# Kernel tuning notes

Hardware: AMD Instinct MI355X
Metric: run time of the kernel (lower is better)

The kernel has to match this reference:

```python
import jax, jax.numpy as jnp
import numpy as np

def _dct_mat():
    k = np.arange(8)[:, None]
    n = np.arange(8)[None, :]
    norm = np.where(k == 0, np.sqrt(1.0 / 8.0), np.sqrt(2.0 / 8.0))
    return jnp.asarray(norm * np.cos(np.pi / 8.0 * (n + 0.5) * k), jnp.float32)

_LUM = np.array([[16,11,10,16,24,40,51,61],[12,12,14,19,26,58,60,55],[14,13,16,24,40,57,69,56],[14,17,22,29,51,87,80,62],[18,22,37,56,68,109,103,77],[24,35,55,64,81,104,113,92],[49,64,78,87,103,121,120,101],[72,92,95,98,112,100,103,99]], np.float32)
_CHROM = np.array([[17,18,24,47,99,99,99,99],[18,21,26,66,99,99,99,99],[24,26,56,99,99,99,99,99],[47,66,99,99,99,99,99,99],[99,99,99,99,99,99,99,99],[99,99,99,99,99,99,99,99],[99,99,99,99,99,99,99,99],[99,99,99,99,99,99,99,99]], np.float32)

def _qtables(quality):
    q = max(1, min(100, int(quality)))
    scale = 5000.0 / q if q < 50 else 200.0 - 2.0 * q
    tbs = np.stack([_LUM, _CHROM]) * scale
    tbs = np.clip((tbs + 50.0) / 100.0, 1.0, 255.0)
    return jnp.asarray(tbs, jnp.float32)

def _jpeg_forward(img, quality):
    bs, _, oh, ow = img.shape
    x = img * 255.0
    pad_h = (8 - oh % 8) % 8
    pad_w = (8 - ow % 8) % 8
    if pad_h or pad_w:
        x = jnp.pad(x, ((0, 0), (0, 0), (0, pad_h), (0, pad_w)), mode='edge')
    h, w = oh + pad_h, ow + pad_w
    W_ycc = jnp.asarray([[0.299, 0.587, 0.114], [-0.1687, -0.3313, 0.5], [0.5, -0.4187, -0.0813]], jnp.float32)
    b_ycc = jnp.asarray([0.0, 128.0, 128.0], jnp.float32)
    # 1x1 conv colorspace transform
    yuv = jnp.einsum('oc,bchw->bohw', W_ycc, x) + b_ycc[None, :, None, None]
    nb = bs * 3
    hb, wb = h // 8, w // 8
    # unfold(kernel=8, stride=8) == non-overlapping 8x8 blocking, block-row-major
    blocks = yuv.reshape(nb, hb, 8, wb, 8).transpose(0, 1, 3, 2, 4).reshape(nb, hb * wb, 8, 8)
    M = _dct_mat()
    dct = jnp.matmul(M, jnp.matmul(blocks - 128.0, M.T))
    qt = _qtables(quality)
    # faithful to original slicing patches_dct[:bs] / [bs:] over the flattened (b,c) dim
    row = jnp.arange(nb)[:, None, None, None]
    qfull = jnp.where(row < bs, qt[0], qt[1])
    t = dct / qfull
    # straight-through round
    tq = (t + jax.lax.stop_gradient(jnp.round(t) - t)) * qfull
    idct = jnp.matmul(M.T, jnp.matmul(tq, M)) + 128.0
    rec = idct.reshape(nb, hb, wb, 8, 8).transpose(0, 1, 3, 2, 4).reshape(bs, 3, h, w)
    rec = rec - b_ycc[None, :, None, None]
    y, cb, cr = rec[:, 0], rec[:, 1], rec[:, 2]
    r = y + 1.402 * cr
    g = y - 0.34414 * cb - 0.71414 * cr
    b = y + 1.772 * cb
    rgb = jnp.stack([r, g, b], axis=1)[:, :, :oh, :ow]
    return jnp.clip(rgb / 255.0, 0.0, 1.0)

def setup_inputs() -> dict:
    key = jax.random.key(0)
    img = jax.random.uniform(key, (16, 3, 512, 512), dtype=jnp.float32)
    return {"img": img, "quality": 80}

def reference(img, quality):
    return _jpeg_forward(img, quality)
```

## Files before the change

### kernel.cpp

```cpp
#include <hip/hip_runtime.h>
#include <math.h>

#define C1 0.9807852804032304
#define C2 0.9238795325112867
#define C3 0.8314696123025452
#define C4 0.7071067811865476
#define C5 0.5555702330196022
#define C6 0.3826834323650898
#define C7 0.19509032201612825
#define N0 0.35355339059327373

static constexpr double Mc[8][8] = {
 {  N0,      N0,      N0,      N0,      N0,      N0,      N0,      N0    },
 {  .5*C1,   .5*C3,   .5*C5,   .5*C7,  -.5*C7,  -.5*C5,  -.5*C3,  -.5*C1 },
 {  .5*C2,   .5*C6,  -.5*C6,  -.5*C2,  -.5*C2,  -.5*C6,   .5*C6,   .5*C2 },
 {  .5*C3,  -.5*C7,  -.5*C1,  -.5*C5,   .5*C5,   .5*C1,   .5*C7,  -.5*C3 },
 {  .5*C4,  -.5*C4,  -.5*C4,   .5*C4,   .5*C4,  -.5*C4,  -.5*C4,   .5*C4 },
 {  .5*C5,  -.5*C1,   .5*C7,   .5*C3,  -.5*C3,  -.5*C7,   .5*C1,  -.5*C5 },
 {  .5*C6,  -.5*C2,   .5*C2,  -.5*C6,  -.5*C6,   .5*C2,  -.5*C2,   .5*C6 },
 {  .5*C7,  -.5*C5,   .5*C3,  -.5*C1,   .5*C1,  -.5*C3,   .5*C5,  -.5*C7 },
};
#define ROWF(r) {(float)Mc[r][0],(float)Mc[r][1],(float)Mc[r][2],(float)Mc[r][3],\
                 (float)Mc[r][4],(float)Mc[r][5],(float)Mc[r][6],(float)Mc[r][7]}
static constexpr float Mcf[8][8] = {ROWF(0),ROWF(1),ROWF(2),ROWF(3),ROWF(4),ROWF(5),ROWF(6),ROWF(7)};

static __device__ const double LUM_BASE[64] = {
 16,11,10,16,24,40,51,61,
 12,12,14,19,26,58,60,55,
 14,13,16,24,40,57,69,56,
 14,17,22,29,51,87,80,62,
 18,22,37,56,68,109,103,77,
 24,35,55,64,81,104,113,92,
 49,64,78,87,103,121,120,101,
 72,92,95,98,112,100,103,99};
static __device__ const double CHROM_BASE[64] = {
 17,18,24,47,99,99,99,99,
 18,21,26,66,99,99,99,99,
 24,26,56,99,99,99,99,99,
 47,66,99,99,99,99,99,99,
 99,99,99,99,99,99,99,99,
 99,99,99,99,99,99,99,99,
 99,99,99,99,99,99,99,99,
 99,99,99,99,99,99,99,99};

__global__ __launch_bounds__(192, 4) void jpeg_fwd(const float* __restrict__ img,
                                                   const int* __restrict__ quality,
                                                   float* __restrict__ out)
{
    __shared__ double QT[128];
    __shared__ double RQ[128];
    __shared__ double U[1728];

    const int t   = threadIdx.x;
    const int w   = t >> 6;
    const int l   = t & 63;
    const int blk = l >> 3;
    const int rr  = l & 7;

    const int b    = blockIdx.x >> 9;
    const int rem  = blockIdx.x & 511;
    const int row0 = (rem >> 3) << 3;
    const int col0 = (rem & 7) << 6;

    const size_t plane = 512 * 512;

    const float* p = img + (size_t)(b * 3) * plane + (size_t)(row0 + rr) * 512 + col0 + blk * 8;
    float4 R0 = *(const float4*)(p);
    float4 R1 = *(const float4*)(p + 4);
    float4 G0 = *(const float4*)(p + plane);
    float4 G1 = *(const float4*)(p + plane + 4);
    float4 B0 = *(const float4*)(p + 2 * plane);
    float4 B1 = *(const float4*)(p + 2 * plane + 4);

    {
        int q = quality[0];
        q = q < 1 ? 1 : (q > 100 ? 100 : q);
        double scale = (q < 50) ? (5000.0 / (double)q) : (200.0 - 2.0 * (double)q);
        #pragma unroll
        for (int h = 0; h < 2; ++h) {
            int e = l + (h << 6);
            int tbl = e >> 6, idx = e & 63;
            double base = tbl ? CHROM_BASE[idx] : LUM_BASE[idx];
            double v = (base * scale + 50.0) / 100.0;
            v = fmin(fmax(v, 1.0), 255.0);
            QT[e] = v;
            RQ[e] = 1.0 / v;
        }
    }

    const double F00 =  0.299 * 255.0,  F01 =  0.587 * 255.0,  F02 =  0.114 * 255.0;
    const double F10 = -0.1687 * 255.0, F11 = -0.3313 * 255.0, F12 =  0.5 * 255.0;
    const double F20 =  0.5 * 255.0,    F21 = -0.4187 * 255.0, F22 = -0.0813 * 255.0;

    float rf[8] = {R0.x, R0.y, R0.z, R0.w, R1.x, R1.y, R1.z, R1.w};
    float gf[8] = {G0.x, G0.y, G0.z, G0.w, G1.x, G1.y, G1.z, G1.w};
    float bf[8] = {B0.x, B0.y, B0.z, B0.w, B1.x, B1.y, B1.z, B1.w};

    double row[8];
    #pragma unroll
    for (int k = 0; k < 8; ++k) {
        double rv = (double)rf[k];
        double gv = (double)gf[k];
        double bv = (double)bf[k];
        double v;
        if (w == 0)      v = F00 * rv + F01 * gv + F02 * bv;
        else if (w == 1) v = F10 * rv + F11 * gv + F12 * bv + 128.0;
        else             v = F20 * rv + F21 * gv + F22 * bv + 128.0;
        row[k] = v - 128.0;
    }

    double y[8];
    {
        double u0[4], v0[4];
        #pragma unroll
        for (int k = 0; k < 4; ++k) {
            u0[k] = row[k] + row[7 - k];
            v0[k] = row[k] - row[7 - k];
        }
        #pragma unroll
        for (int c = 0; c < 8; c += 2) {
            double se = 0.0, so = 0.0;
            #pragma unroll
            for (int k = 0; k < 4; ++k) {
                se += u0[k] * Mc[c][k];
                so += v0[k] * Mc[c + 1][k];
            }
            y[c] = se; y[c + 1] = so;
        }
    }

    {
        double* tb = U + w * 576 + blk * 72 + rr * 9;
        #pragma unroll
        for (int k = 0; k < 8; ++k) tb[k] = y[k];
    }
    double t1[8], qv[8], rv8[8];
    {
        const double* tb = U + w * 576 + blk * 72 + rr;
        #pragma unroll
        for (int k = 0; k < 8; ++k) t1[k] = tb[k * 9];
    }
    const int sel = ((b * 3 + w) < 16) ? 0 : 1;
    #pragma unroll
    for (int j = 0; j < 8; ++j) {
        qv[j]  = QT[(sel << 6) + (j << 3) + rr];
        rv8[j] = RQ[(sel << 6) + (j << 3) + rr];
    }

    double wq[8];
    {
        double tu[4], tv[4];
        #pragma unroll
        for (int k = 0; k < 4; ++k) {
            tu[k] = t1[k] + t1[7 - k];
            tv[k] = t1[k] - t1[7 - k];
        }
        #pragma unroll
        for (int j = 0; j < 8; j += 2) {
            double se = 0.0, so = 0.0;
            #pragma unroll
            for (int k = 0; k < 4; ++k) {
                se += tu[k] * Mc[j][k];
                so += tv[k] * Mc[j + 1][k];
            }
            {
                double q = qv[j], r = rv8[j];
                double qh = se * r;
                double e  = fma(-q, qh, se);
                double qq = fma(e, r, qh);
                wq[j] = rint(qq) * q;
            }
            {
                double q = qv[j + 1], r = rv8[j + 1];
                double qh = so * r;
                double e  = fma(-q, qh, so);
                double qq = fma(e, r, qh);
                wq[j + 1] = rint(qq) * q;
            }
        }
    }

    float wqf[8];
    #pragma unroll
    for (int k = 0; k < 8; ++k) wqf[k] = (float)wq[k];

    float a3[8];
    #pragma unroll
    for (int j = 0; j < 4; ++j) {
        float pe = 0.0f, po = 0.0f;
        #pragma unroll
        for (int k = 0; k < 4; ++k) {
            pe += wqf[2 * k]     * Mcf[2 * k][j];
            po += wqf[2 * k + 1] * Mcf[2 * k + 1][j];
        }
        a3[j]     = pe + po;
        a3[7 - j] = pe - po;
    }

    {
        float* tb = (float*)(U + w * 576) + blk * 72 + rr * 9;
        #pragma unroll
        for (int k = 0; k < 8; ++k) tb[k] = a3[k];
    }
    __syncthreads();

    float tY[8], tU[8], tV[8];
    {
        const float* c0 = (float*)(U + 0 * 576) + blk * 72 + rr;
        const float* c1 = (float*)(U + 1 * 576) + blk * 72 + rr;
        const float* c2 = (float*)(U + 2 * 576) + blk * 72 + rr;
        #pragma unroll
        for (int k = 0; k < 8; ++k) {
            tY[k] = c0[k * 9];
            tU[k] = c1[k * 9];
            tV[k] = c2[k * 9];
        }
    }

    float yr[8], ur[8], vr[8];
    #pragma unroll
    for (int j = 0; j < 4; ++j) {
        float eY = 0.0f, oY = 0.0f, eU = 0.0f, oU = 0.0f, eV = 0.0f, oV = 0.0f;
        #pragma unroll
        for (int k = 0; k < 4; ++k) {
            float me = Mcf[2 * k][j], mo = Mcf[2 * k + 1][j];
            eY += tY[2 * k] * me;  oY += tY[2 * k + 1] * mo;
            eU += tU[2 * k] * me;  oU += tU[2 * k + 1] * mo;
            eV += tV[2 * k] * me;  oV += tV[2 * k + 1] * mo;
        }
        yr[j] = eY + oY;  yr[7 - j] = eY - oY;
        ur[j] = eU + oU;  ur[7 - j] = eU - oU;
        vr[j] = eV + oV;  vr[7 - j] = eV - oV;
    }

    float* q0 = out + (size_t)(b * 3 + w) * plane + (size_t)(row0 + rr) * 512 + col0 + blk * 8;
    float o[8];
    #pragma unroll
    for (int k = 0; k < 8; ++k) {
        float yd = yr[k] + 128.0f;
        float v;
        if (w == 0)      v = yd + 1.402f * vr[k];
        else if (w == 1) v = yd - 0.34414f * ur[k] - 0.71414f * vr[k];
        else             v = yd + 1.772f * ur[k];
        o[k] = fminf(fmaxf(v * (1.0f / 255.0f), 0.0f), 1.0f);
    }
    *(float4*)(q0)     = make_float4(o[0], o[1], o[2], o[3]);
    *(float4*)(q0 + 4) = make_float4(o[4], o[5], o[6], o[7]);
}

extern "C" void kernel_launch(void* const* d_in, const int* in_sizes, int n_in,
                              void* d_out, int out_size, void* d_ws, size_t ws_size,
                              hipStream_t stream) {
    const float* img     = (const float*)d_in[0];
    const int*   quality = (const int*)d_in[1];
    float*       out     = (float*)d_out;
    jpeg_fwd<<<8192, 192, 0, stream>>>(img, quality, out);
}
```

Before: 112.4 us.

## Process all three channels in one wave, replacing block barrier with wave fences

Shrinks each workgroup from three waves (one per color channel) to a single 64-lane wave that processes Y, Cb and Cr in turn, reusing one shared transpose buffer. The __syncthreads is replaced by s_waitcnt lgkmcnt fences, which relies on the whole workgroup being one wave. The aim is to remove block-level barriers and cross-wave LDS exchange. In exchange each wave does three times the serial work with 8192 single-wave blocks, which cuts parallelism per block and may raise register pressure.

```diff
diff --git a/kernel.cpp b/kernel.cpp
--- a/kernel.cpp
+++ b/kernel.cpp
@@ -43,17 +43,18 @@
  99,99,99,99,99,99,99,99,
  99,99,99,99,99,99,99,99};
 
-__global__ __launch_bounds__(192, 4) void jpeg_fwd(const float* __restrict__ img,
-                                                   const int* __restrict__ quality,
-                                                   float* __restrict__ out)
+#define WAVE_FENCE() asm volatile("s_waitcnt lgkmcnt(0)" ::: "memory")
+
+__global__ __launch_bounds__(64, 3) void jpeg_fwd(const float* __restrict__ img,
+                                                  const int* __restrict__ quality,
+                                                  float* __restrict__ out)
 {
     __shared__ double QT[128];
     __shared__ double RQ[128];
-    __shared__ double U[1728];
-
-    const int t   = threadIdx.x;
-    const int w   = t >> 6;
-    const int l   = t & 63;
+    __shared__ double U64[576];
+    __shared__ float  U32[576];
+
+    const int l   = threadIdx.x;
     const int blk = l >> 3;
     const int rr  = l & 7;
 
@@ -87,6 +88,7 @@
             RQ[e] = 1.0 / v;
         }
     }
+    WAVE_FENCE();
 
     const double F00 =  0.299 * 255.0,  F01 =  0.587 * 255.0,  F02 =  0.114 * 255.0;
     const double F10 = -0.1687 * 255.0, F11 = -0.3313 * 255.0, F12 =  0.5 * 255.0;
@@ -96,156 +98,176 @@
     float gf[8] = {G0.x, G0.y, G0.z, G0.w, G1.x, G1.y, G1.z, G1.w};
     float bf[8] = {B0.x, B0.y, B0.z, B0.w, B1.x, B1.y, B1.z, B1.w};
 
-    double row[8];
+    double qv[8], rv8[8];
+    int sel_cur = ((b * 3 + 0) < 16) ? 0 : 1;
+    #pragma unroll
+    for (int j = 0; j < 8; ++j) {
+        qv[j]  = QT[(sel_cur << 6) + (j << 3) + rr];
+        rv8[j] = RQ[(sel_cur << 6) + (j << 3) + rr];
+    }
+
+    float pix0[8], pix1[8], pix2[8];
+
+#define CHANNEL_BODY(CIDX, PIXARR, COLOR_EXPR)                                  \
+    {                                                                           \
+             \
+        int sel_c = ((b * 3 + CIDX) < 16) ? 0 : 1;                              \
+        if (sel_c != sel_cur) {                                                 \
+            sel_cur = sel_c;                                                    \
+            _Pragma("unroll")                                                   \
+            for (int j = 0; j < 8; ++j) {                                       \
+                qv[j]  = QT[(sel_cur << 6) + (j << 3) + rr];                    \
+                rv8[j] = RQ[(sel_cur << 6) + (j << 3) + rr];                    \
+            }                                                                   \
+        }                                                                       \
+           \
+        double row[8];                                                          \
+        _Pragma("unroll")                                                       \
+        for (int k = 0; k < 8; ++k) {                                           \
+            double rv = (double)rf[k];                                          \
+            double gv = (double)gf[k];                                          \
+            double bv = (double)bf[k];                                          \
+            double v  = (COLOR_EXPR);                                           \
+            row[k] = v - 128.0;                                                 \
+        }                                                                       \
+                            \
+        double y[8];                                                            \
+        {                                                                       \
+            double u0[4], v0[4];                                                \
+            _Pragma("unroll")                                                   \
+            for (int k = 0; k < 4; ++k) {                                       \
+                u0[k] = row[k] + row[7 - k];                                    \
+                v0[k] = row[k] - row[7 - k];                                    \
+            }                                                                   \
+            _Pragma("unroll")                                                   \
+            for (int c = 0; c < 8; c += 2) {                                    \
+                double se = 0.0, so = 0.0;                                      \
+                _Pragma("unroll")                                               \
+                for (int k = 0; k < 4; ++k) {                                   \
+                    se += u0[k] * Mc[c][k];                                     \
+                    so += v0[k] * Mc[c + 1][k];                                 \
+                }                                                               \
+                y[c] = se; y[c + 1] = so;                                       \
+            }                                                                   \
+        }                                                                       \
+                            \
+        {                                                                       \
+            double* tb = U64 + blk * 72 + rr * 9;                               \
+            _Pragma("unroll")                                                   \
+            for (int k = 0; k < 8; ++k) tb[k] = y[k];                           \
+        }                                                                       \
+        WAVE_FENCE();                                                           \
+        double t1[8];                                                           \
+        {                                                                       \
+            const double* tb = U64 + blk * 72 + rr;                             \
+            _Pragma("unroll")                                                   \
+            for (int k = 0; k < 8; ++k) t1[k] = tb[k * 9];                      \
+        }                                                                       \
+                \
+        double wq[8];                                                           \
+        {                                                                       \
+            double tu[4], tv[4];                                                \
+            _Pragma("unroll")                                                   \
+            for (int k = 0; k < 4; ++k) {                                       \
+                tu[k] = t1[k] + t1[7 - k];                                      \
+                tv[k] = t1[k] - t1[7 - k];                                      \
+            }                                                                   \
+            _Pragma("unroll")                                                   \
+            for (int j = 0; j < 8; j += 2) {                                    \
+                double se = 0.0, so = 0.0;                                      \
+                _Pragma("unroll")                                               \
+                for (int k = 0; k < 4; ++k) {                                   \
+                    se += tu[k] * Mc[j][k];                                     \
+                    so += tv[k] * Mc[j + 1][k];                                 \
+                }                                                               \
+                {     \
+                    double q = qv[j], r = rv8[j];                               \
+                    double qh = se * r;                                         \
+                    double e  = fma(-q, qh, se);                                \
+                    double qq = fma(e, r, qh);                                  \
+                    wq[j] = rint(qq) * q;                                       \
+                }                                                               \
+                {                                                    \
+                    double q = qv[j + 1], r = rv8[j + 1];                       \
+                    double qh = so * r;                                         \
+                    double e  = fma(-q, qh, so);                                \
+                    double qq = fma(e, r, qh);                                  \
+                    wq[j + 1] = rint(qq) * q;                                   \
+                }                                                               \
+            }                                                                   \
+        }                                                                       \
+                                         \
+        float wqf[8];                                                           \
+        _Pragma("unroll")                                                       \
+        for (int k = 0; k < 8; ++k) wqf[k] = (float)wq[k];                      \
+               \
+        float a3[8];                                                            \
+        _Pragma("unroll")                                                       \
+        for (int j = 0; j < 4; ++j) {                                           \
+            float pe = 0.0f, po = 0.0f;                                         \
+            _Pragma("unroll")                                                   \
+            for (int k = 0; k < 4; ++k) {                                       \
+                pe += wqf[2 * k]     * Mcf[2 * k][j];                           \
+                po += wqf[2 * k + 1] * Mcf[2 * k + 1][j];                       \
+            }                                                                   \
+            a3[j]     = pe + po;                                                \
+            a3[7 - j] = pe - po;                                                \
+        }                                                                       \
+                \
+        {                                                                       \
+            float* tb = U32 + blk * 72 + rr * 9;                                \
+            _Pragma("unroll")                                                   \
+            for (int k = 0; k < 8; ++k) tb[k] = a3[k];                          \
+        }                                                                       \
+        WAVE_FENCE();                                                           \
+        float tC[8];                                                            \
+        {                                                                       \
+            const float* c2 = U32 + blk * 72 + rr;                              \
+            _Pragma("unroll")                                                   \
+            for (int k = 0; k < 8; ++k) tC[k] = c2[k * 9];                      \
+        }                                                                       \
+               \
+        _Pragma("unroll")                                                       \
+        for (int j = 0; j < 4; ++j) {                                           \
+            float e = 0.0f, o = 0.0f;                                           \
+            _Pragma("unroll")                                                   \
+            for (int k = 0; k < 4; ++k) {                                       \
+                e += tC[2 * k]     * Mcf[2 * k][j];                             \
+                o += tC[2 * k + 1] * Mcf[2 * k + 1][j];                         \
+            }                                                                   \
+            PIXARR[j]     = e + o;                                              \
+            PIXARR[7 - j] = e - o;                                              \
+        }                                                                       \
+        WAVE_FENCE();      \
+    }
+
+    CHANNEL_BODY(0, pix0, F00 * rv + F01 * gv + F02 * bv)
+    CHANNEL_BODY(1, pix1, F10 * rv + F11 * gv + F12 * bv + 128.0)
+    CHANNEL_BODY(2, pix2, F20 * rv + F21 * gv + F22 * bv + 128.0)
+#undef CHANNEL_BODY
+
+    float oR[8], oG[8], oB[8];
     #pragma unroll
     for (int k = 0; k < 8; ++k) {
-        double rv = (double)rf[k];
-        double gv = (double)gf[k];
-        double bv = (double)bf[k];
-        double v;
-        if (w == 0)      v = F00 * rv + F01 * gv + F02 * bv;
-        else if (w == 1) v = F10 * rv + F11 * gv + F12 * bv + 128.0;
-        else             v = F20 * rv + F21 * gv + F22 * bv + 128.0;
-        row[k] = v - 128.0;
-    }
-
-    double y[8];
-    {
-        double u0[4], v0[4];
-        #pragma unroll
-        for (int k = 0; k < 4; ++k) {
-            u0[k] = row[k] + row[7 - k];
-            v0[k] = row[k] - row[7 - k];
-        }
-        #pragma unroll
-        for (int c = 0; c < 8; c += 2) {
-            double se = 0.0, so = 0.0;
-            #pragma unroll
-            for (int k = 0; k < 4; ++k) {
-                se += u0[k] * Mc[c][k];
-                so += v0[k] * Mc[c + 1][k];
-            }
-            y[c] = se; y[c + 1] = so;
-        }
-    }
-
-    {
-        double* tb = U + w * 576 + blk * 72 + rr * 9;
-        #pragma unroll
-        for (int k = 0; k < 8; ++k) tb[k] = y[k];
-    }
-    double t1[8], qv[8], rv8[8];
-    {
-        const double* tb = U + w * 576 + blk * 72 + rr;
-        #pragma unroll
-        for (int k = 0; k < 8; ++k) t1[k] = tb[k * 9];
-    }
-    const int sel = ((b * 3 + w) < 16) ? 0 : 1;
-    #pragma unroll
-    for (int j = 0; j < 8; ++j) {
-        qv[j]  = QT[(sel << 6) + (j << 3) + rr];
-        rv8[j] = RQ[(sel << 6) + (j << 3) + rr];
-    }
-
-    double wq[8];
-    {
-        double tu[4], tv[4];
-        #pragma unroll
-        for (int k = 0; k < 4; ++k) {
-            tu[k] = t1[k] + t1[7 - k];
-            tv[k] = t1[k] - t1[7 - k];
-        }
-        #pragma unroll
-        for (int j = 0; j < 8; j += 2) {
-            double se = 0.0, so = 0.0;
-            #pragma unroll
-            for (int k = 0; k < 4; ++k) {
-                se += tu[k] * Mc[j][k];
-                so += tv[k] * Mc[j + 1][k];
-            }
-            {
-                double q = qv[j], r = rv8[j];
-                double qh = se * r;
-                double e  = fma(-q, qh, se);
-                double qq = fma(e, r, qh);
-                wq[j] = rint(qq) * q;
-            }
-            {
-                double q = qv[j + 1], r = rv8[j + 1];
-                double qh = so * r;
-                double e  = fma(-q, qh, so);
-                double qq = fma(e, r, qh);
-                wq[j + 1] = rint(qq) * q;
-            }
-        }
-    }
-
-    float wqf[8];
-    #pragma unroll
-    for (int k = 0; k < 8; ++k) wqf[k] = (float)wq[k];
-
-    float a3[8];
-    #pragma unroll
-    for (int j = 0; j < 4; ++j) {
-        float pe = 0.0f, po = 0.0f;
-        #pragma unroll
-        for (int k = 0; k < 4; ++k) {
-            pe += wqf[2 * k]     * Mcf[2 * k][j];
-            po += wqf[2 * k + 1] * Mcf[2 * k + 1][j];
-        }
-        a3[j]     = pe + po;
-        a3[7 - j] = pe - po;
-    }
-
-    {
-        float* tb = (float*)(U + w * 576) + blk * 72 + rr * 9;
-        #pragma unroll
-        for (int k = 0; k < 8; ++k) tb[k] = a3[k];
-    }
-    __syncthreads();
-
-    float tY[8], tU[8], tV[8];
-    {
-        const float* c0 = (float*)(U + 0 * 576) + blk * 72 + rr;
-        const float* c1 = (float*)(U + 1 * 576) + blk * 72 + rr;
-        const float* c2 = (float*)(U + 2 * 576) + blk * 72 + rr;
-        #pragma unroll
-        for (int k = 0; k < 8; ++k) {
-            tY[k] = c0[k * 9];
-            tU[k] = c1[k * 9];
-            tV[k] = c2[k * 9];
-        }
-    }
-
-    float yr[8], ur[8], vr[8];
-    #pragma unroll
-    for (int j = 0; j < 4; ++j) {
-        float eY = 0.0f, oY = 0.0f, eU = 0.0f, oU = 0.0f, eV = 0.0f, oV = 0.0f;
-        #pragma unroll
-        for (int k = 0; k < 4; ++k) {
-            float me = Mcf[2 * k][j], mo = Mcf[2 * k + 1][j];
-            eY += tY[2 * k] * me;  oY += tY[2 * k + 1] * mo;
-            eU += tU[2 * k] * me;  oU += tU[2 * k + 1] * mo;
-            eV += tV[2 * k] * me;  oV += tV[2 * k + 1] * mo;
-        }
-        yr[j] = eY + oY;  yr[7 - j] = eY - oY;
-        ur[j] = eU + oU;  ur[7 - j] = eU - oU;
-        vr[j] = eV + oV;  vr[7 - j] = eV - oV;
-    }
-
-    float* q0 = out + (size_t)(b * 3 + w) * plane + (size_t)(row0 + rr) * 512 + col0 + blk * 8;
-    float o[8];
-    #pragma unroll
-    for (int k = 0; k < 8; ++k) {
-        float yd = yr[k] + 128.0f;
-        float v;
-        if (w == 0)      v = yd + 1.402f * vr[k];
-        else if (w == 1) v = yd - 0.34414f * ur[k] - 0.71414f * vr[k];
-        else             v = yd + 1.772f * ur[k];
-        o[k] = fminf(fmaxf(v * (1.0f / 255.0f), 0.0f), 1.0f);
-    }
-    *(float4*)(q0)     = make_float4(o[0], o[1], o[2], o[3]);
-    *(float4*)(q0 + 4) = make_float4(o[4], o[5], o[6], o[7]);
+        float yd = pix0[k] + 128.0f;
+        float vR = yd + 1.402f * pix2[k];
+        float vG = yd - 0.34414f * pix1[k] - 0.71414f * pix2[k];
+        float vB = yd + 1.772f * pix1[k];
+        oR[k] = fminf(fmaxf(vR * (1.0f / 255.0f), 0.0f), 1.0f);
+        oG[k] = fminf(fmaxf(vG * (1.0f / 255.0f), 0.0f), 1.0f);
+        oB[k] = fminf(fmaxf(vB * (1.0f / 255.0f), 0.0f), 1.0f);
+    }
+
+    const size_t rowoff = (size_t)(row0 + rr) * 512 + col0 + blk * 8;
+    float* qR = out + (size_t)(b * 3 + 0) * plane + rowoff;
+    float* qG = out + (size_t)(b * 3 + 1) * plane + rowoff;
+    float* qB = out + (size_t)(b * 3 + 2) * plane + rowoff;
+    *(float4*)(qR)     = make_float4(oR[0], oR[1], oR[2], oR[3]);
+    *(float4*)(qR + 4) = make_float4(oR[4], oR[5], oR[6], oR[7]);
+    *(float4*)(qG)     = make_float4(oG[0], oG[1], oG[2], oG[3]);
+    *(float4*)(qG + 4) = make_float4(oG[4], oG[5], oG[6], oG[7]);
+    *(float4*)(qB)     = make_float4(oB[0], oB[1], oB[2], oB[3]);
+    *(float4*)(qB + 4) = make_float4(oB[4], oB[5], oB[6], oB[7]);
 }
 
 extern "C" void kernel_launch(void* const* d_in, const int* in_sizes, int n_in,
@@ -254,5 +276,5 @@
     const float* img     = (const float*)d_in[0];
     const int*   quality = (const int*)d_in[1];
     float*       out     = (float*)d_out;
-    jpeg_fwd<<<8192, 192, 0, stream>>>(img, quality, out);
+    jpeg_fwd<<<8192, 64, 0, stream>>>(img, quality, out);
 }
```

Result: faster. 106.2 us (-5.5%).
